# Performance work log

Hardware: AMD Instinct MI355X
Metric: run time of the kernel (lower is better)

Reference implementation:

```python
import jax, jax.numpy as jnp
import numpy as np

B, S, D, H = 4, 2048, 1024, 16
HD = D // H  # head_dim = 64


def setup_inputs() -> dict:
    key = jax.random.key(0)
    ks = jax.random.split(key, 6)
    sd = 1.0 / np.sqrt(D)
    return {
        "x": jax.random.normal(ks[0], (B, S, D), dtype=jnp.float32),
        "y": jax.random.normal(ks[1], (B, S, D), dtype=jnp.float32),
        "mask": jax.random.normal(ks[2], (1, 1, S, S), dtype=jnp.float32),
        "Wkv": jax.random.normal(ks[3], (D, 2 * D), dtype=jnp.float32) * sd,
        "bkv": jnp.zeros((2 * D,), dtype=jnp.float32),
        "Wq": jax.random.normal(ks[4], (D, D), dtype=jnp.float32) * sd,
        "bq": jnp.zeros((D,), dtype=jnp.float32),
        "Wo": jax.random.normal(ks[5], (D, D), dtype=jnp.float32) * sd,
        "bo": jnp.zeros((D,), dtype=jnp.float32),
    }


def reference(x, y, mask, Wkv, bkv, Wq, bq, Wo, bo):
    b, s, d = x.shape
    kv = x @ Wkv + bkv                      # [B,S,2D]
    q = y @ Wq + bq                         # [B,S,D]
    kv = kv.reshape(b, s, H, 2 * HD).transpose(0, 2, 1, 3)  # [B,H,S,2HD]
    q = q.reshape(b, s, H, HD).transpose(0, 2, 1, 3)        # [B,H,S,HD]
    k, v = kv[..., :HD], kv[..., HD:]
    scaled = jnp.einsum("bhqd,bhkd->bhqk", q, k) / jnp.sqrt(jnp.float32(HD))
    scaled = scaled + mask                  # additive mask, broadcast [1,1,S,S]
    attn = jax.nn.softmax(scaled, axis=-1)
    vals = jnp.einsum("bhqk,bhkd->bhqd", attn, v)  # [B,H,S,HD]
    vals = vals.transpose(0, 2, 1, 3).reshape(b, s, d)
    return vals @ Wo + bo
```

## Files before the change

kernel.cpp:

```cpp
#include <hip/hip_runtime.h>

#define LOG2E 1.44269504088896340736f
#define QSCALE 0.18033688011112042f

typedef __attribute__((ext_vector_type(8))) short bf16x8;
typedef __attribute__((ext_vector_type(4))) float f32x4;

__device__ __forceinline__ unsigned short f2b(float f) {
  union { float f; unsigned int u; } x; x.f = f;
  return (unsigned short)((x.u + 0x8000u) >> 16);
}

__device__ __forceinline__ unsigned int pk_bf16(float a, float b) {
  union { float f; unsigned int u; } xa, xb; xa.f = a; xb.f = b;
  return __builtin_amdgcn_perm(xb.u + 0x8000u, xa.u + 0x8000u, 0x07060302);
}

__device__ __forceinline__ void gld_lds16(const void* g, void* l) {
  __builtin_amdgcn_global_load_lds((const __attribute__((address_space(1))) void*)g,
                                   (__attribute__((address_space(3))) void*)l,
                                   16, 0, 0);
}

__global__ __launch_bounds__(256) void cast_xy(const float* __restrict__ x,
                                               const float* __restrict__ y,
                                               unsigned short* __restrict__ xb,
                                               unsigned short* __restrict__ yb) {
  int i = blockIdx.x * 256 + threadIdx.x;
  const float* in = x; unsigned short* out = xb;
  if (i >= 2097152) { in = y; out = yb; i -= 2097152; }
  float4 v = ((const float4*)in)[i];
  uint2 o;
  o.x = pk_bf16(v.x, v.y);
  o.y = pk_bf16(v.z, v.w);
  ((uint2*)out)[i] = o;
}

__global__ __launch_bounds__(256) void scale_mask(const float* __restrict__ in,
                                                  float* __restrict__ out) {
  int i = blockIdx.x * 256 + threadIdx.x;
  f32x4 v = ((const f32x4*)in)[i];
  ((f32x4*)out)[i] = v * LOG2E;
}

__global__ __launch_bounds__(256) void transpose_cast_all(
    const float* __restrict__ Wkv, const float* __restrict__ Wq,
    const float* __restrict__ Wo, unsigned short* __restrict__ wkvt,
    unsigned short* __restrict__ wqt, unsigned short* __restrict__ wot) {
  __shared__ float t[32][33];
  int tb = blockIdx.x;
  const float* W; unsigned short* Wt; int N;
  if (tb < 2048)      { W = Wkv; Wt = wkvt; N = 2048; }
  else if (tb < 3072) { W = Wq;  Wt = wqt;  N = 1024; tb -= 2048; }
  else                { W = Wo;  Wt = wot;  N = 1024; tb -= 3072; }
  const int K = 1024;
  int tilesN = N >> 5;
  int nb = (tb % tilesN) * 32, kb = (tb / tilesN) * 32;
  int j = threadIdx.x & 31, i0 = threadIdx.x >> 5;
  #pragma unroll
  for (int p = 0; p < 4; ++p) {
    int i = i0 + p * 8;
    t[i][j] = W[(size_t)(kb + i) * N + nb + j];
  }
  __syncthreads();
  #pragma unroll
  for (int p = 0; p < 4; ++p) {
    int i = i0 + p * 8;
    Wt[(size_t)(nb + i) * K + kb + j] = f2b(t[j][i]);
  }
}

template <int MODE>
__global__ __launch_bounds__(256)
void gemm128(const unsigned short* __restrict__ A,
             const unsigned short* __restrict__ Bt,
             const float* __restrict__ bias,
             void* __restrict__ out0, void* __restrict__ out1,
             int M, int N, int K) {
  __shared__ __align__(16) unsigned short As[128 * 64];
  __shared__ __align__(16) unsigned short Bs[128 * 64];
  const int tid = threadIdx.x;
  const int bn = blockIdx.x, bm = blockIdx.y;
  const int wave = tid >> 6, lane = tid & 63;
  const int wm = (wave >> 1) * 64, wn = (wave & 1) * 64;
  const int lrow = lane & 15, quad = lane >> 4;
  const int sw = lrow & 7;

  f32x4 acc[4][4];
  #pragma unroll
  for (int i = 0; i < 4; ++i)
    #pragma unroll
    for (int j = 0; j < 4; ++j)
      #pragma unroll
      for (int r = 0; r < 4; ++r) acc[i][j][r] = 0.f;

  const unsigned short* Ab = A + (size_t)(bm * 128) * K;
  const unsigned short* Bb = Bt + (size_t)(bn * 128) * K;

  for (int k0 = 0; k0 < K; k0 += 64) {
    #pragma unroll
    for (int i = 0; i < 4; ++i) {
      int e = i * 256 + tid;
      int row = e >> 3, gs = (e & 7) ^ (row & 7);
      gld_lds16(Ab + (size_t)row * K + k0 + gs * 8, &As[e * 8]);
    }
    #pragma unroll
    for (int i = 0; i < 4; ++i) {
      int e = i * 256 + tid;
      int row = e >> 3, gs = (e & 7) ^ (row & 7);
      gld_lds16(Bb + (size_t)row * K + k0 + gs * 8, &Bs[e * 8]);
    }
    __builtin_amdgcn_s_waitcnt(0);
    __syncthreads();
    #pragma unroll
    for (int ks = 0; ks < 2; ++ks) {
      bf16x8 af[4], bf[4];
      const int g = ((ks * 4 + quad) ^ sw) * 8;
      #pragma unroll
      for (int i = 0; i < 4; ++i)
        af[i] = *(const bf16x8*)&As[(wm + i * 16 + lrow) * 64 + g];
      #pragma unroll
      for (int j = 0; j < 4; ++j)
        bf[j] = *(const bf16x8*)&Bs[(wn + j * 16 + lrow) * 64 + g];
      #pragma unroll
      for (int i = 0; i < 4; ++i)
        #pragma unroll
        for (int j = 0; j < 4; ++j)
          acc[i][j] = __builtin_amdgcn_mfma_f32_16x16x32_bf16(af[i], bf[j], acc[i][j], 0, 0, 0);
    }
    __syncthreads();
  }

  const int col0 = bn * 128 + wn;
  #pragma unroll
  for (int i = 0; i < 4; ++i) {
    const int row0 = bm * 128 + wm + i * 16 + quad * 4;
    const int b = row0 >> 11, s0 = row0 & 2047;
    #pragma unroll
    for (int j = 0; j < 4; ++j) {
      const int cc = j * 16 + lrow;
      const float bv = bias[col0 + cc];
      float v0 = acc[i][j][0] + bv, v1 = acc[i][j][1] + bv;
      float v2 = acc[i][j][2] + bv, v3 = acc[i][j][3] + bv;
      if (MODE == 0) {
        float* C = (float*)out0;
        size_t off = (size_t)row0 * N + col0 + cc;
        C[off] = v0; C[off + N] = v1; C[off + 2 * N] = v2; C[off + 3 * N] = v3;
      } else if (MODE == 1) {
        const int h = col0 >> 7;
        if ((col0 & 64) == 0) {
          unsigned short* Kb = (unsigned short*)out0;
          size_t base = ((size_t)(b * 16 + h) * 2048 + s0) * 64 + cc;
          Kb[base] = f2b(v0); Kb[base + 64] = f2b(v1);
          Kb[base + 128] = f2b(v2); Kb[base + 192] = f2b(v3);
        } else {
          unsigned short* Vt = (unsigned short*)out1;
          size_t base = ((size_t)(b * 16 + h) * 64 + cc) * 2048 + s0;
          uint2 p; p.x = pk_bf16(v0, v1); p.y = pk_bf16(v2, v3);
          *(uint2*)&Vt[base] = p;
        }
      } else {
        v0 *= QSCALE; v1 *= QSCALE; v2 *= QSCALE; v3 *= QSCALE;
        const int h = col0 >> 6;
        unsigned short* Qb = (unsigned short*)out0;
        size_t base = ((size_t)(b * 16 + h) * 2048 + s0) * 64 + cc;
        Qb[base] = f2b(v0); Qb[base + 64] = f2b(v1);
        Qb[base + 128] = f2b(v2); Qb[base + 192] = f2b(v3);
      }
    }
  }
}

__global__ __launch_bounds__(256)
void attn(const unsigned short* __restrict__ Qbuf,
          const unsigned short* __restrict__ Kbuf,
          const unsigned short* __restrict__ Vtbuf,
          const float* __restrict__ masks,
          unsigned short* __restrict__ vals) {
  const int blk = blockIdx.x;
  const int xcd = blk & 7, slot = blk >> 3;
  const int qt = xcd * 2 + (slot >> 6);
  const int hb = slot & 63;
  const int b = hb >> 4, h = hb & 15;
  const int tid = threadIdx.x, lane = tid & 63, w = tid >> 6;
  const int lrow = lane & 15, quad = lane >> 4;
  const int sw = lrow & 7;

  __shared__ __align__(16) unsigned short Ks[64 * 64];
  __shared__ __align__(16) unsigned short Vs[64 * 64];
  __shared__ __align__(16) unsigned short Ps[128 * 72];

  const unsigned short* qp = Qbuf + ((size_t)(b * 16 + h) * 2048 + qt * 128) * 64;
  const unsigned short* kp = Kbuf + (size_t)(b * 16 + h) * 2048 * 64;
  const unsigned short* vp = Vtbuf + (size_t)(b * 16 + h) * 64 * 2048;
  const float* mp = masks + (size_t)(qt * 128 + w * 32) * 2048;

  #pragma unroll
  for (int i = 0; i < 4; ++i) {
    int e = i * 256 + tid;
    int row = e >> 3, gs = (e & 7) ^ (row & 7);
    gld_lds16(qp + (size_t)row * 64 + gs * 8, &Ps[e * 8]);
  }
  __builtin_amdgcn_s_waitcnt(0);
  __syncthreads();
  bf16x8 qf[2][2];
  #pragma unroll
  for (int iq = 0; iq < 2; ++iq)
    #pragma unroll
    for (int ks = 0; ks < 2; ++ks)
      qf[iq][ks] = *(const bf16x8*)&Ps[(w * 32 + iq * 16 + lrow) * 64 + ((ks * 4 + quad) ^ sw) * 8];
  __syncthreads();

  f32x4 o_acc[4][2];
  #pragma unroll
  for (int id = 0; id < 4; ++id)
    #pragma unroll
    for (int iq = 0; iq < 2; ++iq)
      #pragma unroll
      for (int r = 0; r < 4; ++r) o_acc[id][iq][r] = 0.f;
  float lsum[2] = {0.f, 0.f};

  for (int kt = 0; kt < 32; ++kt) {
    __syncthreads();
    #pragma unroll
    for (int i = 0; i < 2; ++i) {
      int e = i * 256 + tid;
      int row = e >> 3, gs = (e & 7) ^ (row & 7);
      gld_lds16(kp + (size_t)(kt * 64 + row) * 64 + gs * 8, &Ks[e * 8]);
    }
    #pragma unroll
    for (int i = 0; i < 2; ++i) {
      int e = i * 256 + tid;
      int row = e >> 3, gs = (e & 7) ^ (row & 7);
      gld_lds16(vp + (size_t)row * 2048 + kt * 64 + gs * 8, &Vs[e * 8]);
    }
    __builtin_amdgcn_s_waitcnt(0);
    __syncthreads();

    f32x4 z[4][2];
    #pragma unroll
    for (int ik = 0; ik < 4; ++ik)
      #pragma unroll
      for (int iq = 0; iq < 2; ++iq)
        z[ik][iq] = *(const f32x4*)(mp + (size_t)(iq * 16 + lrow) * 2048 + kt * 64 + ik * 16 + quad * 4);

    #pragma unroll
    for (int ks = 0; ks < 2; ++ks) {
      bf16x8 kf[4];
      const int g = ((ks * 4 + quad) ^ sw) * 8;
      #pragma unroll
      for (int ik = 0; ik < 4; ++ik)
        kf[ik] = *(const bf16x8*)&Ks[(ik * 16 + lrow) * 64 + g];
      #pragma unroll
      for (int ik = 0; ik < 4; ++ik)
        #pragma unroll
        for (int iq = 0; iq < 2; ++iq)
          z[ik][iq] = __builtin_amdgcn_mfma_f32_16x16x32_bf16(kf[ik], qf[iq][ks], z[ik][iq], 0, 0, 0);
    }

    #pragma unroll
    for (int ik = 0; ik < 4; ++ik)
      #pragma unroll
      for (int iq = 0; iq < 2; ++iq) {
        float e0 = exp2f(z[ik][iq][0]), e1 = exp2f(z[ik][iq][1]);
        float e2 = exp2f(z[ik][iq][2]), e3 = exp2f(z[ik][iq][3]);
        lsum[iq] += (e0 + e1) + (e2 + e3);
        uint2 p;
        p.x = pk_bf16(e0, e1);
        p.y = pk_bf16(e2, e3);
        *(uint2*)&Ps[(w * 32 + iq * 16 + lrow) * 72 + ik * 16 + quad * 4] = p;
      }
    __builtin_amdgcn_s_waitcnt(0xC07F);

    #pragma unroll
    for (int ks = 0; ks < 2; ++ks) {
      bf16x8 vf[4], pf[2];
      const int g = ((ks * 4 + quad) ^ sw) * 8;
      #pragma unroll
      for (int id = 0; id < 4; ++id)
        vf[id] = *(const bf16x8*)&Vs[(id * 16 + lrow) * 64 + g];
      #pragma unroll
      for (int iq = 0; iq < 2; ++iq)
        pf[iq] = *(const bf16x8*)&Ps[(w * 32 + iq * 16 + lrow) * 72 + ks * 32 + quad * 8];
      #pragma unroll
      for (int id = 0; id < 4; ++id)
        #pragma unroll
        for (int iq = 0; iq < 2; ++iq)
          o_acc[id][iq] = __builtin_amdgcn_mfma_f32_16x16x32_bf16(vf[id], pf[iq], o_acc[id][iq], 0, 0, 0);
    }
  }

  unsigned short* ob = vals + (size_t)(b * 2048 + qt * 128 + w * 32) * 1024 + h * 64;
  #pragma unroll
  for (int iq = 0; iq < 2; ++iq) {
    float s = lsum[iq];
    s += __shfl_xor(s, 16);
    s += __shfl_xor(s, 32);
    float inv = 1.f / s;
    #pragma unroll
    for (int id = 0; id < 4; ++id) {
      uint2 p;
      p.x = pk_bf16(o_acc[id][iq][0] * inv, o_acc[id][iq][1] * inv);
      p.y = pk_bf16(o_acc[id][iq][2] * inv, o_acc[id][iq][3] * inv);
      *(uint2*)&ob[(size_t)(iq * 16 + lrow) * 1024 + id * 16 + quad * 4] = p;
    }
  }
}

extern "C" void kernel_launch(void* const* d_in, const int* in_sizes, int n_in,
                              void* d_out, int out_size, void* d_ws, size_t ws_size,
                              hipStream_t stream) {
  const float* x    = (const float*)d_in[0];
  const float* y    = (const float*)d_in[1];
  const float* mask = (const float*)d_in[2];
  const float* Wkv  = (const float*)d_in[3];
  const float* bkv  = (const float*)d_in[4];
  const float* Wq   = (const float*)d_in[5];
  const float* bq   = (const float*)d_in[6];
  const float* Wo   = (const float*)d_in[7];
  const float* bo   = (const float*)d_in[8];

  char* ws = (char*)d_ws;
  unsigned short* xb    = (unsigned short*)(ws + ((size_t)0 << 20));
  unsigned short* yb    = (unsigned short*)(ws + ((size_t)16 << 20));
  unsigned short* wkvt  = (unsigned short*)(ws + ((size_t)32 << 20));
  unsigned short* wqt   = (unsigned short*)(ws + ((size_t)36 << 20));
  unsigned short* wot   = (unsigned short*)(ws + ((size_t)38 << 20));
  unsigned short* kbuf  = (unsigned short*)(ws + ((size_t)40 << 20));
  unsigned short* vtbuf = (unsigned short*)(ws + ((size_t)56 << 20));
  unsigned short* qbuf  = (unsigned short*)(ws + ((size_t)72 << 20));
  unsigned short* valsb = (unsigned short*)(ws + ((size_t)88 << 20));
  float*          masks = (float*)        (ws + ((size_t)108 << 20));

  cast_xy<<<16384, 256, 0, stream>>>(x, y, xb, yb);
  scale_mask<<<4096, 256, 0, stream>>>(mask, masks);
  transpose_cast_all<<<4096, 256, 0, stream>>>(Wkv, Wq, Wo, wkvt, wqt, wot);

  gemm128<1><<<dim3(16, 64), 256, 0, stream>>>(xb, wkvt, bkv, kbuf, vtbuf, 8192, 2048, 1024);
  gemm128<2><<<dim3(8, 64), 256, 0, stream>>>(yb, wqt, bq, qbuf, nullptr, 8192, 1024, 1024);
  attn<<<1024, 256, 0, stream>>>(qbuf, kbuf, vtbuf, masks, valsb);
  gemm128<0><<<dim3(8, 64), 256, 0, stream>>>(valsb, wot, bo, (float*)d_out, nullptr, 8192, 1024, 1024);
}
```

Before: 463.0 us.

## Switch pipeline to fp16 and restructure attention with 256-row tiles and double-buffered K

After: 467.3 us. Within noise of the previous version (+0.9%).

```diff
diff --git a/kernel.cpp b/kernel.cpp
--- a/kernel.cpp
+++ b/kernel.cpp
@@ -2,18 +2,16 @@
 
 #define LOG2E 1.44269504088896340736f
 #define QSCALE 0.18033688011112042f
-
-typedef __attribute__((ext_vector_type(8))) short bf16x8;
+#define ESHIFT 4.0f
+
+typedef __attribute__((ext_vector_type(8))) _Float16 f16x8;
+typedef __attribute__((ext_vector_type(2))) __fp16 fp16v2;
 typedef __attribute__((ext_vector_type(4))) float f32x4;
 
-__device__ __forceinline__ unsigned short f2b(float f) {
-  union { float f; unsigned int u; } x; x.f = f;
-  return (unsigned short)((x.u + 0x8000u) >> 16);
-}
-
-__device__ __forceinline__ unsigned int pk_bf16(float a, float b) {
-  union { float f; unsigned int u; } xa, xb; xa.f = a; xb.f = b;
-  return __builtin_amdgcn_perm(xb.u + 0x8000u, xa.u + 0x8000u, 0x07060302);
+__device__ __forceinline__ unsigned int pk_f16(float a, float b) {
+  union { fp16v2 h; unsigned int u; } x;
+  x.h = __builtin_amdgcn_cvt_pkrtz(a, b);
+  return x.u;
 }
 
 __device__ __forceinline__ void gld_lds16(const void* g, void* l) {
@@ -24,15 +22,15 @@
 
 __global__ __launch_bounds__(256) void cast_xy(const float* __restrict__ x,
                                                const float* __restrict__ y,
-                                               unsigned short* __restrict__ xb,
-                                               unsigned short* __restrict__ yb) {
+                                               _Float16* __restrict__ xb,
+                                               _Float16* __restrict__ yb) {
   int i = blockIdx.x * 256 + threadIdx.x;
-  const float* in = x; unsigned short* out = xb;
+  const float* in = x; _Float16* out = xb;
   if (i >= 2097152) { in = y; out = yb; i -= 2097152; }
   float4 v = ((const float4*)in)[i];
   uint2 o;
-  o.x = pk_bf16(v.x, v.y);
-  o.y = pk_bf16(v.z, v.w);
+  o.x = pk_f16(v.x, v.y);
+  o.y = pk_f16(v.z, v.w);
   ((uint2*)out)[i] = o;
 }
 
@@ -40,16 +38,16 @@
                                                   float* __restrict__ out) {
   int i = blockIdx.x * 256 + threadIdx.x;
   f32x4 v = ((const f32x4*)in)[i];
-  ((f32x4*)out)[i] = v * LOG2E;
+  ((f32x4*)out)[i] = v * LOG2E - ESHIFT;
 }
 
 __global__ __launch_bounds__(256) void transpose_cast_all(
     const float* __restrict__ Wkv, const float* __restrict__ Wq,
-    const float* __restrict__ Wo, unsigned short* __restrict__ wkvt,
-    unsigned short* __restrict__ wqt, unsigned short* __restrict__ wot) {
+    const float* __restrict__ Wo, _Float16* __restrict__ wkvt,
+    _Float16* __restrict__ wqt, _Float16* __restrict__ wot) {
   __shared__ float t[32][33];
   int tb = blockIdx.x;
-  const float* W; unsigned short* Wt; int N;
+  const float* W; _Float16* Wt; int N;
   if (tb < 2048)      { W = Wkv; Wt = wkvt; N = 2048; }
   else if (tb < 3072) { W = Wq;  Wt = wqt;  N = 1024; tb -= 2048; }
   else                { W = Wo;  Wt = wot;  N = 1024; tb -= 3072; }
@@ -66,19 +64,19 @@
   #pragma unroll
   for (int p = 0; p < 4; ++p) {
     int i = i0 + p * 8;
-    Wt[(size_t)(nb + i) * K + kb + j] = f2b(t[j][i]);
+    Wt[(size_t)(nb + i) * K + kb + j] = (_Float16)t[j][i];
   }
 }
 
 template <int MODE>
 __global__ __launch_bounds__(256)
-void gemm128(const unsigned short* __restrict__ A,
-             const unsigned short* __restrict__ Bt,
+void gemm128(const _Float16* __restrict__ A,
+             const _Float16* __restrict__ Bt,
              const float* __restrict__ bias,
              void* __restrict__ out0, void* __restrict__ out1,
              int M, int N, int K) {
-  __shared__ __align__(16) unsigned short As[128 * 64];
-  __shared__ __align__(16) unsigned short Bs[128 * 64];
+  __shared__ __align__(16) _Float16 As[128 * 64];
+  __shared__ __align__(16) _Float16 Bs[128 * 64];
   const int tid = threadIdx.x;
   const int bn = blockIdx.x, bm = blockIdx.y;
   const int wave = tid >> 6, lane = tid & 63;
@@ -94,8 +92,8 @@
       #pragma unroll
       for (int r = 0; r < 4; ++r) acc[i][j][r] = 0.f;
 
-  const unsigned short* Ab = A + (size_t)(bm * 128) * K;
-  const unsigned short* Bb = Bt + (size_t)(bn * 128) * K;
+  const _Float16* Ab = A + (size_t)(bm * 128) * K;
+  const _Float16* Bb = Bt + (size_t)(bn * 128) * K;
 
   for (int k0 = 0; k0 < K; k0 += 64) {
     #pragma unroll
@@ -114,19 +112,19 @@
     __syncthreads();
     #pragma unroll
     for (int ks = 0; ks < 2; ++ks) {
-      bf16x8 af[4], bf[4];
+      f16x8 af[4], bf[4];
       const int g = ((ks * 4 + quad) ^ sw) * 8;
       #pragma unroll
       for (int i = 0; i < 4; ++i)
-        af[i] = *(const bf16x8*)&As[(wm + i * 16 + lrow) * 64 + g];
+        af[i] = *(const f16x8*)&As[(wm + i * 16 + lrow) * 64 + g];
       #pragma unroll
       for (int j = 0; j < 4; ++j)
-        bf[j] = *(const bf16x8*)&Bs[(wn + j * 16 + lrow) * 64 + g];
+        bf[j] = *(const f16x8*)&Bs[(wn + j * 16 + lrow) * 64 + g];
       #pragma unroll
       for (int i = 0; i < 4; ++i)
         #pragma unroll
         for (int j = 0; j < 4; ++j)
-          acc[i][j] = __builtin_amdgcn_mfma_f32_16x16x32_bf16(af[i], bf[j], acc[i][j], 0, 0, 0);
+          acc[i][j] = __builtin_amdgcn_mfma_f32_16x16x32_f16(af[i], bf[j], acc[i][j], 0, 0, 0);
     }
     __syncthreads();
   }
@@ -149,159 +147,168 @@
       } else if (MODE == 1) {
         const int h = col0 >> 7;
         if ((col0 & 64) == 0) {
-          unsigned short* Kb = (unsigned short*)out0;
+          _Float16* Kb = (_Float16*)out0;
           size_t base = ((size_t)(b * 16 + h) * 2048 + s0) * 64 + cc;
-          Kb[base] = f2b(v0); Kb[base + 64] = f2b(v1);
-          Kb[base + 128] = f2b(v2); Kb[base + 192] = f2b(v3);
+          Kb[base] = (_Float16)v0; Kb[base + 64] = (_Float16)v1;
+          Kb[base + 128] = (_Float16)v2; Kb[base + 192] = (_Float16)v3;
         } else {
-          unsigned short* Vt = (unsigned short*)out1;
+          _Float16* Vt = (_Float16*)out1;
           size_t base = ((size_t)(b * 16 + h) * 64 + cc) * 2048 + s0;
-          uint2 p; p.x = pk_bf16(v0, v1); p.y = pk_bf16(v2, v3);
+          uint2 p; p.x = pk_f16(v0, v1); p.y = pk_f16(v2, v3);
           *(uint2*)&Vt[base] = p;
         }
       } else {
-        v0 *= QSCALE; v1 *= QSCALE; v2 *= QSCALE; v3 *= QSCALE;
         const int h = col0 >> 6;
-        unsigned short* Qb = (unsigned short*)out0;
+        _Float16* Qb = (_Float16*)out0;
         size_t base = ((size_t)(b * 16 + h) * 2048 + s0) * 64 + cc;
-        Qb[base] = f2b(v0); Qb[base + 64] = f2b(v1);
-        Qb[base + 128] = f2b(v2); Qb[base + 192] = f2b(v3);
+        Qb[base] = (_Float16)(v0 * QSCALE); Qb[base + 64] = (_Float16)(v1 * QSCALE);
+        Qb[base + 128] = (_Float16)(v2 * QSCALE); Qb[base + 192] = (_Float16)(v3 * QSCALE);
       }
     }
   }
 }
 
-__global__ __launch_bounds__(256)
-void attn(const unsigned short* __restrict__ Qbuf,
-          const unsigned short* __restrict__ Kbuf,
-          const unsigned short* __restrict__ Vtbuf,
+__global__ __launch_bounds__(256, 2)
+void attn(const _Float16* __restrict__ Qbuf,
+          const _Float16* __restrict__ Kbuf,
+          const _Float16* __restrict__ Vtbuf,
           const float* __restrict__ masks,
-          unsigned short* __restrict__ vals) {
+          _Float16* __restrict__ vals) {
   const int blk = blockIdx.x;
-  const int xcd = blk & 7, slot = blk >> 3;
-  const int qt = xcd * 2 + (slot >> 6);
-  const int hb = slot & 63;
+  const int xcd = blk & 7, s = blk >> 3;
+  const int qt2 = s & 7;
+  const int hb = (s >> 3) * 8 + xcd;
   const int b = hb >> 4, h = hb & 15;
   const int tid = threadIdx.x, lane = tid & 63, w = tid >> 6;
   const int lrow = lane & 15, quad = lane >> 4;
   const int sw = lrow & 7;
 
-  __shared__ __align__(16) unsigned short Ks[64 * 64];
-  __shared__ __align__(16) unsigned short Vs[64 * 64];
-  __shared__ __align__(16) unsigned short Ps[128 * 72];
-
-  const unsigned short* qp = Qbuf + ((size_t)(b * 16 + h) * 2048 + qt * 128) * 64;
-  const unsigned short* kp = Kbuf + (size_t)(b * 16 + h) * 2048 * 64;
-  const unsigned short* vp = Vtbuf + (size_t)(b * 16 + h) * 64 * 2048;
-  const float* mp = masks + (size_t)(qt * 128 + w * 32) * 2048;
-
-  #pragma unroll
-  for (int i = 0; i < 4; ++i) {
+  __shared__ __align__(16) _Float16 Ks[2][64 * 64];
+  __shared__ __align__(16) _Float16 Ps[256 * 72];
+
+  const _Float16* qp = Qbuf + ((size_t)hb * 2048 + qt2 * 256) * 64;
+  const _Float16* kp = Kbuf + (size_t)hb * 2048 * 64;
+  const _Float16* vp = Vtbuf + (size_t)hb * 64 * 2048;
+  const float* mp = masks + (size_t)(qt2 * 256 + w * 64) * 2048;
+
+  #pragma unroll
+  for (int i = 0; i < 8; ++i) {
     int e = i * 256 + tid;
     int row = e >> 3, gs = (e & 7) ^ (row & 7);
     gld_lds16(qp + (size_t)row * 64 + gs * 8, &Ps[e * 8]);
   }
-  __builtin_amdgcn_s_waitcnt(0);
+  #pragma unroll
+  for (int i = 0; i < 2; ++i) {
+    int e = i * 256 + tid;
+    int row = e >> 3, gs = (e & 7) ^ (row & 7);
+    gld_lds16(kp + (size_t)row * 64 + gs * 8, &Ks[0][e * 8]);
+  }
   __syncthreads();
-  bf16x8 qf[2][2];
-  #pragma unroll
-  for (int iq = 0; iq < 2; ++iq)
+
+  f16x8 qf[4][2];
+  #pragma unroll
+  for (int iq = 0; iq < 4; ++iq)
     #pragma unroll
     for (int ks = 0; ks < 2; ++ks)
-      qf[iq][ks] = *(const bf16x8*)&Ps[(w * 32 + iq * 16 + lrow) * 64 + ((ks * 4 + quad) ^ sw) * 8];
-  __syncthreads();
-
-  f32x4 o_acc[4][2];
+      qf[iq][ks] = *(const f16x8*)&Ps[(w * 64 + iq * 16 + lrow) * 64 + ((ks * 4 + quad) ^ sw) * 8];
+  __builtin_amdgcn_s_waitcnt(0xC07F);
+
+  f16x8 ones;
+  {
+    _Float16 o = (lrow == 0) ? (_Float16)1.0f : (_Float16)0.0f;
+    #pragma unroll
+    for (int r = 0; r < 8; ++r) ones[r] = o;
+  }
+
+  f32x4 o_acc[4][4];
+  f32x4 o_l[4];
   #pragma unroll
   for (int id = 0; id < 4; ++id)
     #pragma unroll
-    for (int iq = 0; iq < 2; ++iq)
+    for (int iq = 0; iq < 4; ++iq)
       #pragma unroll
       for (int r = 0; r < 4; ++r) o_acc[id][iq][r] = 0.f;
-  float lsum[2] = {0.f, 0.f};
+  #pragma unroll
+  for (int iq = 0; iq < 4; ++iq)
+    #pragma unroll
+    for (int r = 0; r < 4; ++r) o_l[iq][r] = 0.f;
 
   for (int kt = 0; kt < 32; ++kt) {
-    __syncthreads();
-    #pragma unroll
-    for (int i = 0; i < 2; ++i) {
-      int e = i * 256 + tid;
-      int row = e >> 3, gs = (e & 7) ^ (row & 7);
-      gld_lds16(kp + (size_t)(kt * 64 + row) * 64 + gs * 8, &Ks[e * 8]);
-    }
-    #pragma unroll
-    for (int i = 0; i < 2; ++i) {
-      int e = i * 256 + tid;
-      int row = e >> 3, gs = (e & 7) ^ (row & 7);
-      gld_lds16(vp + (size_t)row * 2048 + kt * 64 + gs * 8, &Vs[e * 8]);
-    }
-    __builtin_amdgcn_s_waitcnt(0);
-    __syncthreads();
-
-    f32x4 z[4][2];
-    #pragma unroll
-    for (int ik = 0; ik < 4; ++ik)
-      #pragma unroll
-      for (int iq = 0; iq < 2; ++iq)
-        z[ik][iq] = *(const f32x4*)(mp + (size_t)(iq * 16 + lrow) * 2048 + kt * 64 + ik * 16 + quad * 4);
+    const int cur = kt & 1;
+    __builtin_amdgcn_s_barrier();
+    if (kt < 31) {
+      #pragma unroll
+      for (int i = 0; i < 2; ++i) {
+        int e = i * 256 + tid;
+        int row = e >> 3, gs = (e & 7) ^ (row & 7);
+        gld_lds16(kp + (size_t)((kt + 1) * 64 + row) * 64 + gs * 8, &Ks[cur ^ 1][e * 8]);
+      }
+      __builtin_amdgcn_s_waitcnt(0xF72);
+    } else {
+      __builtin_amdgcn_s_waitcnt(0xF70);
+    }
+    __builtin_amdgcn_s_barrier();
+
+    f16x8 vfr[2][4];
+    #pragma unroll
+    for (int ks = 0; ks < 2; ++ks)
+      #pragma unroll
+      for (int id = 0; id < 4; ++id)
+        vfr[ks][id] = *(const f16x8*)(vp + (size_t)(id * 16 + lrow) * 2048 + kt * 64 + ks * 32 + quad * 8);
+
+    #pragma unroll
+    for (int ik = 0; ik < 4; ++ik) {
+      f16x8 kf0 = *(const f16x8*)&Ks[cur][(ik * 16 + lrow) * 64 + ((quad) ^ sw) * 8];
+      f16x8 kf1 = *(const f16x8*)&Ks[cur][(ik * 16 + lrow) * 64 + ((4 + quad) ^ sw) * 8];
+      f32x4 z[4];
+      #pragma unroll
+      for (int iq = 0; iq < 4; ++iq)
+        z[iq] = *(const f32x4*)(mp + (size_t)(iq * 16 + lrow) * 2048 + kt * 64 + ik * 16 + quad * 4);
+      #pragma unroll
+      for (int iq = 0; iq < 4; ++iq)
+        z[iq] = __builtin_amdgcn_mfma_f32_16x16x32_f16(kf0, qf[iq][0], z[iq], 0, 0, 0);
+      #pragma unroll
+      for (int iq = 0; iq < 4; ++iq)
+        z[iq] = __builtin_amdgcn_mfma_f32_16x16x32_f16(kf1, qf[iq][1], z[iq], 0, 0, 0);
+      #pragma unroll
+      for (int iq = 0; iq < 4; ++iq) {
+        float e0 = exp2f(z[iq][0]), e1 = exp2f(z[iq][1]);
+        float e2 = exp2f(z[iq][2]), e3 = exp2f(z[iq][3]);
+        uint2 p;
+        p.x = pk_f16(e0, e1);
+        p.y = pk_f16(e2, e3);
+        *(uint2*)&Ps[(w * 64 + iq * 16 + lrow) * 72 + ik * 16 + quad * 4] = p;
+      }
+    }
+    __builtin_amdgcn_s_waitcnt(0xC07F);
 
     #pragma unroll
     for (int ks = 0; ks < 2; ++ks) {
-      bf16x8 kf[4];
-      const int g = ((ks * 4 + quad) ^ sw) * 8;
-      #pragma unroll
-      for (int ik = 0; ik < 4; ++ik)
-        kf[ik] = *(const bf16x8*)&Ks[(ik * 16 + lrow) * 64 + g];
-      #pragma unroll
-      for (int ik = 0; ik < 4; ++ik)
-        #pragma unroll
-        for (int iq = 0; iq < 2; ++iq)
-          z[ik][iq] = __builtin_amdgcn_mfma_f32_16x16x32_bf16(kf[ik], qf[iq][ks], z[ik][iq], 0, 0, 0);
-    }
-
-    #pragma unroll
-    for (int ik = 0; ik < 4; ++ik)
-      #pragma unroll
-      for (int iq = 0; iq < 2; ++iq) {
-        float e0 = exp2f(z[ik][iq][0]), e1 = exp2f(z[ik][iq][1]);
-        float e2 = exp2f(z[ik][iq][2]), e3 = exp2f(z[ik][iq][3]);
-        lsum[iq] += (e0 + e1) + (e2 + e3);
-        uint2 p;
-        p.x = pk_bf16(e0, e1);
-        p.y = pk_bf16(e2, e3);
-        *(uint2*)&Ps[(w * 32 + iq * 16 + lrow) * 72 + ik * 16 + quad * 4] = p;
-      }
-    __builtin_amdgcn_s_waitcnt(0xC07F);
-
-    #pragma unroll
-    for (int ks = 0; ks < 2; ++ks) {
-      bf16x8 vf[4], pf[2];
-      const int g = ((ks * 4 + quad) ^ sw) * 8;
-      #pragma unroll
-      for (int id = 0; id < 4; ++id)
-        vf[id] = *(const bf16x8*)&Vs[(id * 16 + lrow) * 64 + g];
-      #pragma unroll
-      for (int iq = 0; iq < 2; ++iq)
-        pf[iq] = *(const bf16x8*)&Ps[(w * 32 + iq * 16 + lrow) * 72 + ks * 32 + quad * 8];
+      f16x8 pf[4];
+      #pragma unroll
+      for (int iq = 0; iq < 4; ++iq)
+        pf[iq] = *(const f16x8*)&Ps[(w * 64 + iq * 16 + lrow) * 72 + ks * 32 + quad * 8];
       #pragma unroll
       for (int id = 0; id < 4; ++id)
         #pragma unroll
-        for (int iq = 0; iq < 2; ++iq)
-          o_acc[id][iq] = __builtin_amdgcn_mfma_f32_16x16x32_bf16(vf[id], pf[iq], o_acc[id][iq], 0, 0, 0);
-    }
-  }
-
-  unsigned short* ob = vals + (size_t)(b * 2048 + qt * 128 + w * 32) * 1024 + h * 64;
-  #pragma unroll
-  for (int iq = 0; iq < 2; ++iq) {
-    float s = lsum[iq];
-    s += __shfl_xor(s, 16);
-    s += __shfl_xor(s, 32);
-    float inv = 1.f / s;
+        for (int iq = 0; iq < 4; ++iq)
+          o_acc[id][iq] = __builtin_amdgcn_mfma_f32_16x16x32_f16(vfr[ks][id], pf[iq], o_acc[id][iq], 0, 0, 0);
+      #pragma unroll
+      for (int iq = 0; iq < 4; ++iq)
+        o_l[iq] = __builtin_amdgcn_mfma_f32_16x16x32_f16(ones, pf[iq], o_l[iq], 0, 0, 0);
+    }
+  }
+
+  _Float16* ob = vals + (size_t)(b * 2048 + qt2 * 256 + w * 64) * 1024 + h * 64;
+  #pragma unroll
+  for (int iq = 0; iq < 4; ++iq) {
+    float l = __shfl(o_l[iq][0], lrow);
+    float inv = 1.f / l;
     #pragma unroll
     for (int id = 0; id < 4; ++id) {
       uint2 p;
-      p.x = pk_bf16(o_acc[id][iq][0] * inv, o_acc[id][iq][1] * inv);
-      p.y = pk_bf16(o_acc[id][iq][2] * inv, o_acc[id][iq][3] * inv);
+      p.x = pk_f16(o_acc[id][iq][0] * inv, o_acc[id][iq][1] * inv);
+      p.y = pk_f16(o_acc[id][iq][2] * inv, o_acc[id][iq][3] * inv);
       *(uint2*)&ob[(size_t)(iq * 16 + lrow) * 1024 + id * 16 + quad * 4] = p;
     }
   }
@@ -321,16 +328,16 @@
   const float* bo   = (const float*)d_in[8];
 
   char* ws = (char*)d_ws;
-  unsigned short* xb    = (unsigned short*)(ws + ((size_t)0 << 20));
-  unsigned short* yb    = (unsigned short*)(ws + ((size_t)16 << 20));
-  unsigned short* wkvt  = (unsigned short*)(ws + ((size_t)32 << 20));
-  unsigned short* wqt   = (unsigned short*)(ws + ((size_t)36 << 20));
-  unsigned short* wot   = (unsigned short*)(ws + ((size_t)38 << 20));
-  unsigned short* kbuf  = (unsigned short*)(ws + ((size_t)40 << 20));
-  unsigned short* vtbuf = (unsigned short*)(ws + ((size_t)56 << 20));
-  unsigned short* qbuf  = (unsigned short*)(ws + ((size_t)72 << 20));
-  unsigned short* valsb = (unsigned short*)(ws + ((size_t)88 << 20));
-  float*          masks = (float*)        (ws + ((size_t)108 << 20));
+  _Float16* xb    = (_Float16*)(ws + ((size_t)0 << 20));
+  _Float16* yb    = (_Float16*)(ws + ((size_t)16 << 20));
+  _Float16* wkvt  = (_Float16*)(ws + ((size_t)32 << 20));
+  _Float16* wqt   = (_Float16*)(ws + ((size_t)36 << 20));
+  _Float16* wot   = (_Float16*)(ws + ((size_t)38 << 20));
+  _Float16* kbuf  = (_Float16*)(ws + ((size_t)40 << 20));
+  _Float16* vtbuf = (_Float16*)(ws + ((size_t)56 << 20));
+  _Float16* qbuf  = (_Float16*)(ws + ((size_t)72 << 20));
+  _Float16* valsb = (_Float16*)(ws + ((size_t)88 << 20));
+  float*    masks = (float*)   (ws + ((size_t)108 << 20));
 
   cast_xy<<<16384, 256, 0, stream>>>(x, y, xb, yb);
   scale_mask<<<4096, 256, 0, stream>>>(mask, masks);
@@ -338,6 +345,6 @@
 
   gemm128<1><<<dim3(16, 64), 256, 0, stream>>>(xb, wkvt, bkv, kbuf, vtbuf, 8192, 2048, 1024);
   gemm128<2><<<dim3(8, 64), 256, 0, stream>>>(yb, wqt, bq, qbuf, nullptr, 8192, 1024, 1024);
-  attn<<<1024, 256, 0, stream>>>(qbuf, kbuf, vtbuf, masks, valsb);
+  attn<<<512, 256, 0, stream>>>(qbuf, kbuf, vtbuf, masks, valsb);
   gemm128<0><<<dim3(8, 64), 256, 0, stream>>>(valsb, wot, bo, (float*)d_out, nullptr, 8192, 1024, 1024);
 }
```
